# Kernel optimization log

Measured on AMD Instinct MI355X. Metric: run time of the kernel, lower is better.

Reference implementation:

```python
import jax, jax.numpy as jnp
import numpy as np

C = 256      # channels (multiple of 32 for GroupNorm)
K = 3        # kernel
PAD = 1      # padding
G = 32       # GroupNorm groups
EPS = 1e-5


def setup_inputs() -> dict:
    key = jax.random.key(0)
    ks = jax.random.split(key, 7)
    B, H, W = 4, 64, 64
    return {
        "x": jax.random.normal(ks[0], (B, C, H, W), jnp.float32),
        "offset": jax.random.normal(ks[1], (B, 2 * K * K, H, W), jnp.float32),
        "weight": jax.random.normal(ks[2], (C, C, K, K), jnp.float32) * 0.01,
        "att_w": jax.random.normal(ks[3], (1, C), jnp.float32) * 0.01,
        "att_b": jnp.zeros((1,), jnp.float32),
        "gamma": jnp.ones((C,), jnp.float32),
        "beta": jnp.zeros((C,), jnp.float32),
    }


def _bilinear_one(xb, py, px):
    # xb: [C, H, W]; py, px: [KK, H, W] fractional sample coords (zero-pad outside)
    H, W = xb.shape[1], xb.shape[2]
    y0 = jnp.floor(py)
    x0 = jnp.floor(px)
    y1 = y0 + 1.0
    x1 = x0 + 1.0
    wy1 = py - y0
    wy0 = 1.0 - wy1
    wx1 = px - x0
    wx0 = 1.0 - wx1

    def g(yi, xi):
        valid = (yi >= 0) & (yi < H) & (xi >= 0) & (xi < W)
        yc = jnp.clip(yi, 0, H - 1).astype(jnp.int32)
        xc = jnp.clip(xi, 0, W - 1).astype(jnp.int32)
        return xb[:, yc, xc] * valid[None].astype(xb.dtype)  # [C, KK, H, W]

    return (g(y0, x0) * (wy0 * wx0)[None] + g(y0, x1) * (wy0 * wx1)[None]
            + g(y1, x0) * (wy1 * wx0)[None] + g(y1, x1) * (wy1 * wx1)[None])


def reference(x, offset, weight, att_w, att_b, gamma, beta):
    B, Cc, H, W = x.shape
    KK = K * K
    off = offset.reshape(B, KK, 2, H, W)  # (dy, dx) per kernel tap
    ii, jj = jnp.meshgrid(jnp.arange(K), jnp.arange(K), indexing='ij')
    dky = (ii - PAD).reshape(KK).astype(x.dtype)
    dkx = (jj - PAD).reshape(KK).astype(x.dtype)
    ys = jnp.arange(H, dtype=x.dtype)
    xs = jnp.arange(W, dtype=x.dtype)
    # sample coords [B, KK, H, W]
    py = ys[None, :, None] + dky[:, None, None] + off[:, :, 0]
    px = xs[None, None, :] + dkx[:, None, None] + off[:, :, 1]

    # deformable unfold: [B, C, KK, H, W]
    xu = jax.vmap(_bilinear_one)(x, py, px)

    # max over kernel taps -> channel attention gate
    xm = xu.max(axis=2)  # [B, C, H, W]
    att = jax.nn.sigmoid(jnp.einsum('bchw,oc->bohw', xm, att_w)
                         + att_b[None, :, None, None])  # [B, 1, H, W]

    # gate the unfolded samples, then emulate the conv as one GEMM
    xw = xu * att[:, :, None]  # broadcast over C, KK
    cols = xw.transpose(1, 2, 0, 3, 4).reshape(Cc * KK, B * H * W)  # [C*KK, BHW]
    out = (weight.reshape(Cc, Cc * KK) @ cols).reshape(Cc, B, H, W).transpose(1, 0, 2, 3)

    # GroupNorm(32, C) + ReLU
    og = out.reshape(B, G, Cc // G, H, W)
    mu = og.mean(axis=(2, 3, 4), keepdims=True)
    var = og.var(axis=(2, 3, 4), keepdims=True)
    on = ((og - mu) * jax.lax.rsqrt(var + EPS)).reshape(B, Cc, H, W)
    return jax.nn.relu(on * gamma[None, :, None, None] + beta[None, :, None, None])
```

## Files before the change

kernel.cpp:

```cpp
#include <hip/hip_runtime.h>

#define CT 256
#define KDIM 2304
#define COLP 296
#define CSZ (32 * COLP)

typedef unsigned short u16;
typedef _Float16 h2 __attribute__((ext_vector_type(2)));
typedef _Float16 h8 __attribute__((ext_vector_type(8)));
typedef __attribute__((ext_vector_type(4))) float f32x4;

__device__ __forceinline__ unsigned pkh(float a, float b) {
    h2 r; r[0] = (_Float16)a; r[1] = (_Float16)b;
    return __builtin_bit_cast(unsigned, r);
}

__global__ __launch_bounds__(256) void k_prep(const float* __restrict__ x, uint4* __restrict__ xi,
                                              const float* __restrict__ wgt, uint4* __restrict__ pw)
{
    if (blockIdx.x < 2048) {
        int u = blockIdx.x * 256 + threadIdx.x;
        int bcg = u >> 12, p = u & 4095;
        const float* xp = x + (((size_t)bcg) << 15) + p;
        unsigned r[4];
#pragma unroll
        for (int i = 0; i < 4; ++i)
            r[i] = pkh(xp[(size_t)(2 * i) << 12], xp[(size_t)(2 * i + 1) << 12]);
        uint4 o; o.x = r[0]; o.y = r[1]; o.z = r[2]; o.w = r[3];
        xi[u] = o;
    } else {
        int u = (blockIdx.x - 2048) * 256 + threadIdx.x;
        int kc = u >> 10, rm = u & 1023;
        int m = rm >> 2, j = rm & 3;
        int round = kc / 9, tap = kc - round * 9;
        const float* src = wgt + (size_t)m * KDIM + tap;
        int c0 = round * 32 + j * 8;
        unsigned q[4];
#pragma unroll
        for (int i = 0; i < 4; ++i)
            q[i] = pkh(src[(size_t)(c0 + 2 * i) * 9], src[(size_t)(c0 + 2 * i + 1) * 9]);
        uint4 o; o.x = q[0]; o.y = q[1]; o.z = q[2]; o.w = q[3];
        pw[u] = o;
    }
}

struct GB {
    uint4 c00, c01, c10, c11;
    unsigned wx, wy;
    int dst;
};

__device__ __forceinline__ void g_load(int it, int round, size_t xib,
                                       const uint2* s_wt, const int2* s_off,
                                       const uint4* __restrict__ xi, GB& g)
{
    int sp = it / 288;
    int rem = it - sp * 288;
    uint2 wp = s_wt[rem];
    int2 of = s_off[rem];
    g.wx = wp.x; g.wy = wp.y;
    const uint4* gp = xi + xib + ((size_t)((round << 2) + sp) << 12);
    g.c00 = gp[of.x & 0xffff];
    g.c01 = gp[(of.x >> 16) & 0xffff];
    g.c10 = gp[of.y & 0xffff];
    g.c11 = gp[(of.y >> 16) & 0xffff];
    g.dst = (rem & 31) * COLP + (rem >> 5) * 32 + (sp << 3);
}

__device__ __forceinline__ void g_fin(const GB& g, u16* colb)
{
    h2 w01 = __builtin_bit_cast(h2, g.wx);
    h2 w23 = __builtin_bit_cast(h2, g.wy);
    h2 wxp = (h2){w01[0], w01[0]}, wyp = (h2){w01[1], w01[1]};
    h2 wzp = (h2){w23[0], w23[0]}, wwp = (h2){w23[1], w23[1]};
    const unsigned* a00 = (const unsigned*)&g.c00;
    const unsigned* a01 = (const unsigned*)&g.c01;
    const unsigned* a10 = (const unsigned*)&g.c10;
    const unsigned* a11 = (const unsigned*)&g.c11;
    unsigned o[4];
#pragma unroll
    for (int q = 0; q < 4; ++q) {
        h2 rr = wxp * __builtin_bit_cast(h2, a00[q]) + wyp * __builtin_bit_cast(h2, a01[q])
              + wzp * __builtin_bit_cast(h2, a10[q]) + wwp * __builtin_bit_cast(h2, a11[q]);
        o[q] = __builtin_bit_cast(unsigned, rr);
    }
    uint4 ov; ov.x = o[0]; ov.y = o[1]; ov.z = o[2]; ov.w = o[3];
    *(uint4*)&colb[g.dst] = ov;
}

__global__ __launch_bounds__(512, 4) void k_main(const uint4* __restrict__ xi, const float* __restrict__ off,
                                                 const uint4* __restrict__ pw, const float* __restrict__ att_w,
                                                 const float* __restrict__ att_b,
                                                 float* __restrict__ outp, float* __restrict__ gnpart)
{
    __shared__ uint2 s_wt[288];
    __shared__ int2 s_off[288];
    __shared__ u16 col[2 * CSZ];
    __shared__ float s_att[32];

    int rowblk = blockIdx.x >> 1, half = blockIdx.x & 1;
    int b = rowblk >> 6, h = rowblk & 63, n0 = half * 32;
    int tid = threadIdx.x;
    int lane = tid & 63, w = tid >> 6;
    int l15 = lane & 15, kb = lane >> 4;
    int wm = w * 32;
    int nn_a = w * 4 + (lane >> 4);
    int ca = (lane & 15) * 2;

    for (int e = tid; e < 288; e += 512) {
        int kk = e >> 5, wl = e & 31;
        int ww_ = n0 + wl;
        int ky = kk / 3, kx = kk - ky * 3;
        float dy = off[((size_t)(b * 18 + 2 * kk) * 64 + h) * 64 + ww_];
        float dx = off[((size_t)(b * 18 + 2 * kk + 1) * 64 + h) * 64 + ww_];
        float py = (float)(h + ky - 1) + dy;
        float px = (float)(ww_ + kx - 1) + dx;
        float y0f = floorf(py), x0f = floorf(px);
        int y0 = (int)y0f, x0 = (int)x0f;
        float fy = py - y0f, fx = px - x0f;
        float vy0 = (y0 >= 0 && y0 < 64) ? 1.f : 0.f;
        float vy1 = (y0 >= -1 && y0 < 63) ? 1.f : 0.f;
        float vx0 = (x0 >= 0 && x0 < 64) ? 1.f : 0.f;
        float vx1 = (x0 >= -1 && x0 < 63) ? 1.f : 0.f;
        float w0 = (1.f - fy) * (1.f - fx) * vy0 * vx0;
        float w1 = (1.f - fy) * fx * vy0 * vx1;
        float w2 = fy * (1.f - fx) * vy1 * vx0;
        float w3 = fy * fx * vy1 * vx1;
        uint2 wp;
        wp.x = pkh(w0, w1);
        wp.y = pkh(w2, w3);
        int yc0 = min(max(y0, 0), 63), yc1 = min(max(y0 + 1, 0), 63);
        int xc0 = min(max(x0, 0), 63), xc1 = min(max(x0 + 1, 0), 63);
        s_wt[e] = wp;
        s_off[e] = make_int2((yc0 * 64 + xc0) | ((yc0 * 64 + xc1) << 16),
                             (yc1 * 64 + xc0) | ((yc1 * 64 + xc1) << 16));
    }

    size_t xib = (size_t)(b * 32) << 12;

    float att_acc = 0.f;
    f32x4 acc[2][2];
#pragma unroll
    for (int mt = 0; mt < 2; ++mt)
#pragma unroll
        for (int nt = 0; nt < 2; ++nt) acc[mt][nt] = (f32x4){0.f, 0.f, 0.f, 0.f};

    int pwoff[2];
#pragma unroll
    for (int mt = 0; mt < 2; ++mt) pwoff[mt] = (wm + mt * 16 + l15) * 4 + kb;

    __syncthreads();

    {
        GB g0, g1;
        g_load(tid, 0, xib, s_wt, s_off, xi, g0);
        g_load(tid + 512, 0, xib, s_wt, s_off, xi, g1);
        g_fin(g0, col);
        g_fin(g1, col);
        if (tid < 128) {
            GB g2;
            g_load(tid + 1024, 0, xib, s_wt, s_off, xi, g2);
            g_fin(g2, col);
        }
    }

    uint4 aa[4][2];
#pragma unroll
    for (int ts = 0; ts < 4; ++ts)
#pragma unroll
        for (int mt = 0; mt < 2; ++mt)
            aa[ts][mt] = pw[(size_t)ts * 1024 + pwoff[mt]];

    __syncthreads();

    for (int r = 0; r < 8; ++r) {
        u16* cb = col + (r & 1) * CSZ;
        u16* nb = col + ((r & 1) ^ 1) * CSZ;

        GB g0, g1, g2;
        if (r < 7) g_load(tid, r + 1, xib, s_wt, s_off, xi, g0);

        {
            int spa = ca >> 3, co = ca & 7;
            const u16* base = &cb[nn_a * COLP + spa * 8 + co];
            float m0 = -1e30f, m1 = -1e30f;
#pragma unroll
            for (int t = 0; t < 9; ++t) {
                unsigned v = *(const unsigned*)(base + t * 32);
                h2 vv = __builtin_bit_cast(h2, v);
                m0 = fmaxf(m0, (float)vv[0]);
                m1 = fmaxf(m1, (float)vv[1]);
            }
            int cbx = r * 32 + ca;
            att_acc += att_w[cbx] * m0 + att_w[cbx + 1] * m1;
        }

#pragma unroll
        for (int ts = 0; ts < 9; ++ts) {
            h8 bf[2];
#pragma unroll
            for (int nt = 0; nt < 2; ++nt)
                bf[nt] = *(const h8*)&cb[(nt * 16 + l15) * COLP + ts * 32 + kb * 8];
            h8 af[2];
#pragma unroll
            for (int mt = 0; mt < 2; ++mt) af[mt] = __builtin_bit_cast(h8, aa[ts & 3][mt]);
            if (ts + 4 < 9) {
#pragma unroll
                for (int mt = 0; mt < 2; ++mt)
                    aa[ts & 3][mt] = pw[(size_t)(r * 9 + ts + 4) * 1024 + pwoff[mt]];
            } else if (r < 7) {
                int tsp = (ts == 8) ? 0 : (ts - 4);
#pragma unroll
                for (int mt = 0; mt < 2; ++mt)
                    aa[tsp][mt] = pw[(size_t)((r + 1) * 9 + tsp) * 1024 + pwoff[mt]];
            }
#pragma unroll
            for (int mt = 0; mt < 2; ++mt)
#pragma unroll
                for (int nt = 0; nt < 2; ++nt)
                    acc[mt][nt] = __builtin_amdgcn_mfma_f32_16x16x32_f16(af[mt], bf[nt], acc[mt][nt], 0, 0, 0);
            if (ts == 2 && r < 7) {
                g_fin(g0, nb);
                g_load(tid + 512, r + 1, xib, s_wt, s_off, xi, g1);
            }
            if (ts == 5 && r < 7) {
                g_fin(g1, nb);
                if (tid < 128) g_load(tid + 1024, r + 1, xib, s_wt, s_off, xi, g2);
            }
        }
        if (r < 7 && tid < 128) g_fin(g2, nb);
        __syncthreads();
    }

#pragma unroll
    for (int d = 1; d <= 8; d <<= 1) att_acc += __shfl_xor(att_acc, d);
    if ((lane & 15) == 0) s_att[nn_a] = 1.f / (1.f + expf(-(att_acc + att_b[0])));
    __syncthreads();

    float attn[2];
#pragma unroll
    for (int nt = 0; nt < 2; ++nt) attn[nt] = s_att[nt * 16 + l15];

#pragma unroll
    for (int mt = 0; mt < 2; ++mt) {
        float s1 = 0.f, s2 = 0.f;
#pragma unroll
        for (int nt = 0; nt < 2; ++nt)
#pragma unroll
            for (int r = 0; r < 4; ++r) {
                float v = acc[mt][nt][r] * attn[nt];
                int m = wm + mt * 16 + kb * 4 + r;
                outp[(((size_t)(b * CT + m)) << 12) + h * 64 + n0 + nt * 16 + l15] = v;
                s1 += v; s2 += v * v;
            }
#pragma unroll
        for (int d = 1; d <= 16; d <<= 1) {
            s1 += __shfl_xor(s1, d);
            s2 += __shfl_xor(s2, d);
        }
        if ((lane & 31) == 0) {
            int gidx = w * 4 + mt * 2 + (kb >> 1);
            gnpart[blockIdx.x * 64 + gidx * 2] = s1;
            gnpart[blockIdx.x * 64 + gidx * 2 + 1] = s2;
        }
    }
}

__global__ __launch_bounds__(256) void k_gn(const float* __restrict__ gnpart, const float* __restrict__ gamma,
                                            const float* __restrict__ beta, float* __restrict__ outp)
{
    __shared__ float rs1[128], rs2[128];
    __shared__ float s_stat[2];
    int bg = blockIdx.x;
    int b = bg >> 5, g = bg & 31;
    int tid = threadIdx.x;
    if (tid < 128) {
        int blk = (b * 64 + (tid >> 1)) * 2 + (tid & 1);
        rs1[tid] = gnpart[blk * 64 + g * 2];
        rs2[tid] = gnpart[blk * 64 + g * 2 + 1];
    }
    __syncthreads();
    if (tid < 64) {
        float a = rs1[tid] + rs1[tid + 64];
        float c = rs2[tid] + rs2[tid + 64];
#pragma unroll
        for (int d = 1; d <= 32; d <<= 1) {
            a += __shfl_xor(a, d);
            c += __shfl_xor(c, d);
        }
        if (tid == 0) {
            float mean = a * (1.f / 32768.f);
            float var = c * (1.f / 32768.f) - mean * mean;
            s_stat[0] = mean;
            s_stat[1] = rsqrtf(var + 1e-5f);
        }
    }
    __syncthreads();
    float mean = s_stat[0], rstd = s_stat[1];
    float4* p4 = (float4*)(outp + ((size_t)(b * CT + g * 8) << 12));
    for (int i = tid; i < 8192; i += 256) {
        int c = g * 8 + (i >> 10);
        float ga = gamma[c], be = beta[c];
        float4 v = p4[i];
        float4 r;
        r.x = fmaxf((v.x - mean) * rstd * ga + be, 0.f);
        r.y = fmaxf((v.y - mean) * rstd * ga + be, 0.f);
        r.z = fmaxf((v.z - mean) * rstd * ga + be, 0.f);
        r.w = fmaxf((v.w - mean) * rstd * ga + be, 0.f);
        p4[i] = r;
    }
}

extern "C" void kernel_launch(void* const* d_in, const int* in_sizes, int n_in,
                              void* d_out, int out_size, void* d_ws, size_t ws_size,
                              hipStream_t stream)
{
    const float* x = (const float*)d_in[0];
    const float* off = (const float*)d_in[1];
    const float* wgt = (const float*)d_in[2];
    const float* attw = (const float*)d_in[3];
    const float* attb = (const float*)d_in[4];
    const float* gamma = (const float*)d_in[5];
    const float* beta = (const float*)d_in[6];
    float* outp = (float*)d_out;

    char* ws = (char*)d_ws;
    uint4* xi = (uint4*)ws;
    uint4* pw = (uint4*)(ws + 8388608);
    float* gnpart = (float*)(ws + 9568256);

    k_prep<<<dim3(2336), dim3(256), 0, stream>>>(x, xi, wgt, pw);
    k_main<<<dim3(512), dim3(512), 0, stream>>>(xi, off, pw, attw, attb, outp, gnpart);
    k_gn<<<dim3(128), dim3(256), 0, stream>>>(gnpart, gamma, beta, outp);
}
```

Measured before the change: 168.7 us.

## Restructure col tile layout, remap blocks per XCD, shorten weight prefetch ring

Result: faster. 163.8 us (-2.9%).

```diff
diff --git a/kernel.cpp b/kernel.cpp
--- a/kernel.cpp
+++ b/kernel.cpp
@@ -2,8 +2,7 @@
 
 #define CT 256
 #define KDIM 2304
-#define COLP 296
-#define CSZ (32 * COLP)
+#define CSZ2 9216
 
 typedef unsigned short u16;
 typedef _Float16 h2 __attribute__((ext_vector_type(2)));
@@ -61,10 +60,10 @@
     g.wx = wp.x; g.wy = wp.y;
     const uint4* gp = xi + xib + ((size_t)((round << 2) + sp) << 12);
     g.c00 = gp[of.x & 0xffff];
-    g.c01 = gp[(of.x >> 16) & 0xffff];
+    g.c01 = gp[(unsigned)of.x >> 16];
     g.c10 = gp[of.y & 0xffff];
-    g.c11 = gp[(of.y >> 16) & 0xffff];
-    g.dst = (rem & 31) * COLP + (rem >> 5) * 32 + (sp << 3);
+    g.c11 = gp[(unsigned)of.y >> 16];
+    g.dst = it * 8;
 }
 
 __device__ __forceinline__ void g_fin(const GB& g, u16* colb)
@@ -95,11 +94,17 @@
 {
     __shared__ uint2 s_wt[288];
     __shared__ int2 s_off[288];
-    __shared__ u16 col[2 * CSZ];
+    __shared__ u16 col[2 * CSZ2];
     __shared__ float s_att[32];
 
-    int rowblk = blockIdx.x >> 1, half = blockIdx.x & 1;
-    int b = rowblk >> 6, h = rowblk & 63, n0 = half * 32;
+    int bid = blockIdx.x;
+    int xcd = bid & 7, idx = bid >> 3;
+    int b = xcd >> 1;
+    int local = ((xcd & 1) << 6) + idx;
+    int h = local >> 1, half = local & 1;
+    int lbid = b * 128 + local;
+    int n0 = half * 32;
+
     int tid = threadIdx.x;
     int lane = tid & 63, w = tid >> 6;
     int l15 = lane & 15, kb = lane >> 4;
@@ -152,21 +157,18 @@
     __syncthreads();
 
     {
-        GB g0, g1;
+        GB g0, g1, g2;
         g_load(tid, 0, xib, s_wt, s_off, xi, g0);
         g_load(tid + 512, 0, xib, s_wt, s_off, xi, g1);
         g_fin(g0, col);
+        if (tid < 128) g_load(tid + 1024, 0, xib, s_wt, s_off, xi, g2);
         g_fin(g1, col);
-        if (tid < 128) {
-            GB g2;
-            g_load(tid + 1024, 0, xib, s_wt, s_off, xi, g2);
-            g_fin(g2, col);
-        }
-    }
-
-    uint4 aa[4][2];
-#pragma unroll
-    for (int ts = 0; ts < 4; ++ts)
+        if (tid < 128) g_fin(g2, col);
+    }
+
+    uint4 aa[3][2];
+#pragma unroll
+    for (int ts = 0; ts < 3; ++ts)
 #pragma unroll
         for (int mt = 0; mt < 2; ++mt)
             aa[ts][mt] = pw[(size_t)ts * 1024 + pwoff[mt]];
@@ -174,19 +176,19 @@
     __syncthreads();
 
     for (int r = 0; r < 8; ++r) {
-        u16* cb = col + (r & 1) * CSZ;
-        u16* nb = col + ((r & 1) ^ 1) * CSZ;
+        u16* cb = col + (r & 1) * CSZ2;
+        u16* nb = col + ((r & 1) ^ 1) * CSZ2;
 
         GB g0, g1, g2;
         if (r < 7) g_load(tid, r + 1, xib, s_wt, s_off, xi, g0);
 
         {
             int spa = ca >> 3, co = ca & 7;
-            const u16* base = &cb[nn_a * COLP + spa * 8 + co];
+            const u16* base = &cb[spa * 2304 + nn_a * 8 + co];
             float m0 = -1e30f, m1 = -1e30f;
 #pragma unroll
             for (int t = 0; t < 9; ++t) {
-                unsigned v = *(const unsigned*)(base + t * 32);
+                unsigned v = *(const unsigned*)(base + t * 256);
                 h2 vv = __builtin_bit_cast(h2, v);
                 m0 = fmaxf(m0, (float)vv[0]);
                 m1 = fmaxf(m1, (float)vv[1]);
@@ -200,26 +202,25 @@
             h8 bf[2];
 #pragma unroll
             for (int nt = 0; nt < 2; ++nt)
-                bf[nt] = *(const h8*)&cb[(nt * 16 + l15) * COLP + ts * 32 + kb * 8];
+                bf[nt] = *(const h8*)&cb[kb * 2304 + ts * 256 + (nt * 16 + l15) * 8];
             h8 af[2];
 #pragma unroll
-            for (int mt = 0; mt < 2; ++mt) af[mt] = __builtin_bit_cast(h8, aa[ts & 3][mt]);
-            if (ts + 4 < 9) {
+            for (int mt = 0; mt < 2; ++mt) af[mt] = __builtin_bit_cast(h8, aa[ts % 3][mt]);
+            if (ts + 3 < 9) {
 #pragma unroll
                 for (int mt = 0; mt < 2; ++mt)
-                    aa[ts & 3][mt] = pw[(size_t)(r * 9 + ts + 4) * 1024 + pwoff[mt]];
+                    aa[ts % 3][mt] = pw[(size_t)(r * 9 + ts + 3) * 1024 + pwoff[mt]];
             } else if (r < 7) {
-                int tsp = (ts == 8) ? 0 : (ts - 4);
 #pragma unroll
                 for (int mt = 0; mt < 2; ++mt)
-                    aa[tsp][mt] = pw[(size_t)((r + 1) * 9 + tsp) * 1024 + pwoff[mt]];
+                    aa[ts % 3][mt] = pw[(size_t)((r + 1) * 9 + (ts - 6)) * 1024 + pwoff[mt]];
             }
 #pragma unroll
             for (int mt = 0; mt < 2; ++mt)
 #pragma unroll
                 for (int nt = 0; nt < 2; ++nt)
                     acc[mt][nt] = __builtin_amdgcn_mfma_f32_16x16x32_f16(af[mt], bf[nt], acc[mt][nt], 0, 0, 0);
-            if (ts == 2 && r < 7) {
+            if (ts == 1 && r < 7) {
                 g_fin(g0, nb);
                 g_load(tid + 512, r + 1, xib, s_wt, s_off, xi, g1);
             }
@@ -260,8 +261,8 @@
         }
         if ((lane & 31) == 0) {
             int gidx = w * 4 + mt * 2 + (kb >> 1);
-            gnpart[blockIdx.x * 64 + gidx * 2] = s1;
-            gnpart[blockIdx.x * 64 + gidx * 2 + 1] = s2;
+            gnpart[lbid * 64 + gidx * 2] = s1;
+            gnpart[lbid * 64 + gidx * 2 + 1] = s2;
         }
     }
 }
```
